# Performance work log

Measured on AMD Instinct MI355X. Metric: run time of the kernel, lower is better.

Reference implementation:

```python
import jax, jax.numpy as jnp
import numpy as np

T = 65536
INPUT_SIZE = 128
HIDDEN = 100
OUT = 1


def setup_inputs() -> dict:
    key = jax.random.key(0)
    ks = jax.random.split(key, 8)
    s = 1.0 / np.sqrt(HIDDEN)  # PyTorch LSTM/Linear init bound
    u = lambda k, shape: jax.random.uniform(k, shape, jnp.float32, -s, s)
    return {
        "input_x": jax.random.normal(ks[0], (T, INPUT_SIZE), jnp.float32),
        "W_ih": u(ks[1], (4 * HIDDEN, INPUT_SIZE)),
        "W_hh": u(ks[2], (4 * HIDDEN, HIDDEN)),
        "b_ih": u(ks[3], (4 * HIDDEN,)),
        "b_hh": u(ks[4], (4 * HIDDEN,)),
        "W_lin": u(ks[5], (OUT, HIDDEN)),
        "b_lin": u(ks[6], (OUT,)),
    }


def reference(input_x, W_ih, W_hh, b_ih, b_hh, W_lin, b_lin):
    H = W_hh.shape[1]
    # batch=1: squeeze it away; precompute input projections for all timesteps
    x_proj = input_x @ W_ih.T + (b_ih + b_hh)  # [T, 4H]

    def step(carry, xp):
        h, c = carry
        gates = xp + h @ W_hh.T  # [4H]
        i, f, g, o = jnp.split(gates, 4)
        i = jax.nn.sigmoid(i)
        f = jax.nn.sigmoid(f)
        g = jnp.tanh(g)
        o = jax.nn.sigmoid(o)
        c = f * c + i * g
        h = o * jnp.tanh(c)
        return (h, c), h

    h0 = jnp.zeros((H,), input_x.dtype)
    c0 = jnp.zeros((H,), input_x.dtype)
    _, hs = jax.lax.scan(step, (h0, c0), x_proj)  # hs: [T, H]
    predictions = jax.nn.sigmoid(hs @ W_lin.T + b_lin)  # [T, 1]
    return predictions
```

## Files before the change

### kernel.cpp

```cpp
#include <hip/hip_runtime.h>
#include <hip/hip_bf16.h>

#define TSEQ 65536
#define INPUT_SIZE 128
#define HIDDEN 100
#define GATES 400

typedef __attribute__((ext_vector_type(8))) short bf16x8;
typedef __attribute__((ext_vector_type(4))) float f32x4;

__device__ __forceinline__ unsigned short f2bf(float x) {
    union { float f; unsigned int u; } v; v.f = x;
    unsigned int r = v.u + 0x7fffu + ((v.u >> 16) & 1u);
    return (unsigned short)(r >> 16);
}
__device__ __forceinline__ unsigned short f2bf_fast(float x) {
    unsigned int r;
    asm("v_cvt_pk_bf16_f32 %0, %1, %2" : "=v"(r) : "v"(x), "v"(0.0f));
    return (unsigned short)r;
}
__device__ __forceinline__ float bf2f(unsigned int u) {
    union { unsigned int u; float f; } v; v.u = u << 16; return v.f;
}
__device__ __forceinline__ float rcp_fast(float x) { return __builtin_amdgcn_rcpf(x); }
__device__ __forceinline__ float sigm(float x) { return rcp_fast(1.0f + __expf(-x)); }

template <int CTRL>
__device__ __forceinline__ float qb(float v) {
    int i = __builtin_bit_cast(int, v);
    int r = __builtin_amdgcn_mov_dpp(i, CTRL, 0xF, 0xF, true);
    return __builtin_bit_cast(float, r);
}

#define LDS_BARRIER()                                              \
    do {                                                           \
        asm volatile("s_waitcnt lgkmcnt(0)" ::: "memory");         \
        __builtin_amdgcn_s_barrier();                              \
        asm volatile("" ::: "memory");                             \
    } while (0)

__global__ __launch_bounds__(256) void xproj_kernel(
    const float* __restrict__ x,
    const float* __restrict__ W,
    const float* __restrict__ bi,
    const float* __restrict__ bh,
    float* __restrict__ xp)
{
    __shared__ __align__(16) float xs[16 * 128];
    const int tid = threadIdx.x;
    const int t0 = blockIdx.x * 16;

#pragma unroll
    for (int i = 0; i < 8; ++i)
        xs[i * 256 + tid] = x[(size_t)t0 * 128 + i * 256 + tid];
    __syncthreads();

    const int j1 = tid;
    const int j2 = tid + 256;
    const bool has2 = (j2 < GATES);
    const int u1 = j1 % 100, g1 = j1 / 100;
    const int p1 = 16 * (u1 >> 2) + 4 * (u1 & 3) + g1;
    const int u2 = has2 ? (j2 % 100) : 0, g2 = has2 ? (j2 / 100) : 0;
    const int p2 = 16 * (u2 >> 2) + 4 * (u2 & 3) + g2;

    float acc1[16], acc2[16];
    const float bias1 = bi[j1] + bh[j1];
    const float bias2 = has2 ? (bi[j2] + bh[j2]) : 0.0f;
#pragma unroll
    for (int tt = 0; tt < 16; ++tt) { acc1[tt] = bias1; acc2[tt] = bias2; }

    const float4* W4 = reinterpret_cast<const float4*>(W);
    const float4* xs4 = reinterpret_cast<const float4*>(xs);

    for (int kk = 0; kk < 32; ++kk) {
        const float4 wa = W4[(size_t)j1 * 32 + kk];
        float4 wb = make_float4(0.f, 0.f, 0.f, 0.f);
        if (has2) wb = W4[(size_t)j2 * 32 + kk];
#pragma unroll
        for (int tt = 0; tt < 16; ++tt) {
            const float4 xv = xs4[tt * 32 + kk];
            acc1[tt] = fmaf(wa.x, xv.x, acc1[tt]);
            acc1[tt] = fmaf(wa.y, xv.y, acc1[tt]);
            acc1[tt] = fmaf(wa.z, xv.z, acc1[tt]);
            acc1[tt] = fmaf(wa.w, xv.w, acc1[tt]);
            acc2[tt] = fmaf(wb.x, xv.x, acc2[tt]);
            acc2[tt] = fmaf(wb.y, xv.y, acc2[tt]);
            acc2[tt] = fmaf(wb.z, xv.z, acc2[tt]);
            acc2[tt] = fmaf(wb.w, xv.w, acc2[tt]);
        }
    }

#pragma unroll
    for (int tt = 0; tt < 16; ++tt) {
        xp[(size_t)(t0 + tt) * GATES + p1] = acc1[tt];
        if (has2) xp[(size_t)(t0 + tt) * GATES + p2] = acc2[tt];
    }
}

__global__ __launch_bounds__(512, 1) void lstm_rec_kernel(
    const float* __restrict__ xp,
    const float* __restrict__ Whh,
    unsigned short* __restrict__ hs)
{
    __shared__ __align__(16) unsigned short h_lds[2][128];

    const int tid = threadIdx.x;
    const int lane = tid & 63;
    const int w = tid >> 6;
    const int bq = lane >> 4;
    const int m = lane & 15;
    const int g = m & 3;

    bf16x8 wfrag[4][4];
#pragma unroll
    for (int i = 0; i < 4; ++i) {
        const int ti = (i < 3) ? (3 * w + i) : 24;
        const bool valid = (i < 3) || (w == 7);
        const int uu = 4 * ti + (m >> 2);
        const int orow = g * 100 + uu;
#pragma unroll
        for (int kk = 0; kk < 4; ++kk) {
            float vals[8];
            if (valid && kk < 3) {
                const float4 w0 = *(const float4*)&Whh[(size_t)orow * 100 + kk * 32 + bq * 8];
                const float4 w1 = *(const float4*)&Whh[(size_t)orow * 100 + kk * 32 + bq * 8 + 4];
                vals[0] = w0.x; vals[1] = w0.y; vals[2] = w0.z; vals[3] = w0.w;
                vals[4] = w1.x; vals[5] = w1.y; vals[6] = w1.z; vals[7] = w1.w;
            } else if (valid && bq == 0) {
                const float4 w0 = *(const float4*)&Whh[(size_t)orow * 100 + 96];
                vals[0] = w0.x; vals[1] = w0.y; vals[2] = w0.z; vals[3] = w0.w;
                vals[4] = 0.f; vals[5] = 0.f; vals[6] = 0.f; vals[7] = 0.f;
            } else {
#pragma unroll
                for (int j = 0; j < 8; ++j) vals[j] = 0.f;
            }
#pragma unroll
            for (int j = 0; j < 8; ++j) wfrag[i][kk][j] = (short)f2bf(vals[j]);
        }
    }

    const int mytile = (bq < 3) ? (3 * w + bq) : 24;
    const int unit = 4 * mytile + (m >> 2);
    const int pown = 16 * mytile + m;
    const bool qvalid = (bq < 3) || (w == 7);
    const bool writer = qvalid && (g == 3);
    const float kk2 = (g == 2) ? 2.0f : 1.0f;
    const float bsub = (g == 2) ? 2.0f : 1.0f;
    const bool isg1 = (g == 1);

    if (tid < 128) { h_lds[0][tid] = 0; h_lds[1][tid] = 0; }
    float c = 0.0f;
    float xqv[4];
#pragma unroll
    for (int p = 0; p < 4; ++p)
        xqv[p] = xp[(size_t)p * GATES + pown];
    __syncthreads();

    for (int t = 0; t < TSEQ; t += 4) {
#pragma unroll
        for (int u = 0; u < 4; ++u) {
            const int tt = t + u;
            const int cur = u & 1;

            bf16x8 bfr[4];
#pragma unroll
            for (int kk = 0; kk < 4; ++kk) {
                const uint4 braw = *(const uint4*)&h_lds[cur][kk * 32 + bq * 8];
                bfr[kk] = __builtin_bit_cast(bf16x8, braw);
            }

            f32x4 acc_s[4];
#pragma unroll
            for (int i = 0; i < 4; ++i) {
                if (i < 3 || w == 7) {
                    f32x4 acc = {0.f, 0.f, 0.f, 0.f};
                    acc = __builtin_amdgcn_mfma_f32_16x16x32_bf16(bfr[0], wfrag[i][0], acc, 0, 0, 0);
                    acc = __builtin_amdgcn_mfma_f32_16x16x32_bf16(bfr[1], wfrag[i][1], acc, 0, 0, 0);
                    acc = __builtin_amdgcn_mfma_f32_16x16x32_bf16(bfr[2], wfrag[i][2], acc, 0, 0, 0);
                    acc = __builtin_amdgcn_mfma_f32_16x16x32_bf16(bfr[3], wfrag[i][3], acc, 0, 0, 0);
                    acc_s[i] = acc;
                } else {
                    acc_s[i] = (f32x4){0.f, 0.f, 0.f, 0.f};
                }
            }

            float pre = acc_s[0][0];
            pre = (bq == 1) ? acc_s[1][0] : pre;
            pre = (bq == 2) ? acc_s[2][0] : pre;
            pre = (bq == 3) ? acc_s[3][0] : pre;
            pre += xqv[u];

            const float e = __expf(pre * kk2);
            const float act = fmaf(-bsub, rcp_fast(e + 1.0f), 1.0f);

            const float prod = act * qb<0xAA>(act);
            const float cnew = fmaf(act, c, qb<0x00>(prod));
            c = isg1 ? cnew : c;
            const float e2 = __expf(c + c);
            const float tc = fmaf(-2.0f, rcp_fast(e2 + 1.0f), 1.0f);
            const float hv = act * qb<0x55>(tc);
            const unsigned short hb = f2bf_fast(hv);

            if (writer) {
                h_lds[1 - cur][unit] = hb;
                hs[(size_t)tt * HIDDEN + unit] = hb;
            }
            xqv[u] = xp[(size_t)(tt + 4) * GATES + pown];

            LDS_BARRIER();
        }
    }
}

__global__ __launch_bounds__(256) void pred_kernel(
    const unsigned short* __restrict__ hs,
    const float* __restrict__ wlin,
    const float* __restrict__ blin,
    float* __restrict__ out)
{
    __shared__ __align__(16) float wl[HIDDEN];
    const int tid = threadIdx.x;
    if (tid < HIDDEN) wl[tid] = wlin[tid];
    __syncthreads();

    const int t = blockIdx.x * 256 + tid;
    const unsigned short* hrow = hs + (size_t)t * HIDDEN;
    float acc = blin[0];
#pragma unroll
    for (int kk = 0; kk < 25; ++kk) {
        const uint2 v = *(const uint2*)&hrow[kk * 4];
        acc = fmaf(bf2f(v.x & 0xffffu), wl[kk * 4 + 0], acc);
        acc = fmaf(bf2f(v.x >> 16),     wl[kk * 4 + 1], acc);
        acc = fmaf(bf2f(v.y & 0xffffu), wl[kk * 4 + 2], acc);
        acc = fmaf(bf2f(v.y >> 16),     wl[kk * 4 + 3], acc);
    }
    out[t] = sigm(acc);
}

extern "C" void kernel_launch(void* const* d_in, const int* in_sizes, int n_in,
                              void* d_out, int out_size, void* d_ws, size_t ws_size,
                              hipStream_t stream) {
    const float* x     = (const float*)d_in[0];
    const float* W_ih  = (const float*)d_in[1];
    const float* W_hh  = (const float*)d_in[2];
    const float* b_ih  = (const float*)d_in[3];
    const float* b_hh  = (const float*)d_in[4];
    const float* W_lin = (const float*)d_in[5];
    const float* b_lin = (const float*)d_in[6];
    float* out = (float*)d_out;

    float* xp = (float*)d_ws;
    unsigned short* hs = (unsigned short*)(xp + (size_t)TSEQ * GATES);

    xproj_kernel<<<TSEQ / 16, 256, 0, stream>>>(x, W_ih, b_ih, b_hh, xp);
    lstm_rec_kernel<<<1, 512, 0, stream>>>(xp, W_hh, hs);
    pred_kernel<<<TSEQ / 256, 256, 0, stream>>>(hs, W_lin, b_lin, out);
}
```

Baseline: 23.44 ms.

## Replace MFMA recurrent matvec with per-lane fp16 dot2 over register-resident weights

The per-step recurrent matvec moves off MFMA tiles and onto plain VALU work. Each lane owns one gate row of W_hh, held in 50 fp16x2 registers, and computes its dot product against the whole h vector read from LDS using v_dot2 instructions. The hidden state and the stored hs switch from bf16 to fp16, and the xproj output layout becomes a simple 4*unit+gate interleave. The aim is to cut per-step MFMA latency and the lane-select overhead on the serial critical path. The cost is 13 LDS vector reads per lane per step and a longer serial dot2 chain.

```diff
diff --git a/kernel.cpp b/kernel.cpp
--- a/kernel.cpp
+++ b/kernel.cpp
@@ -6,24 +6,20 @@
 #define HIDDEN 100
 #define GATES 400
 
-typedef __attribute__((ext_vector_type(8))) short bf16x8;
-typedef __attribute__((ext_vector_type(4))) float f32x4;
-
-__device__ __forceinline__ unsigned short f2bf(float x) {
-    union { float f; unsigned int u; } v; v.f = x;
-    unsigned int r = v.u + 0x7fffu + ((v.u >> 16) & 1u);
-    return (unsigned short)(r >> 16);
-}
-__device__ __forceinline__ unsigned short f2bf_fast(float x) {
-    unsigned int r;
-    asm("v_cvt_pk_bf16_f32 %0, %1, %2" : "=v"(r) : "v"(x), "v"(0.0f));
-    return (unsigned short)r;
-}
-__device__ __forceinline__ float bf2f(unsigned int u) {
-    union { unsigned int u; float f; } v; v.u = u << 16; return v.f;
-}
+typedef __fp16 __attribute__((ext_vector_type(2))) f16x2;
+
 __device__ __forceinline__ float rcp_fast(float x) { return __builtin_amdgcn_rcpf(x); }
 __device__ __forceinline__ float sigm(float x) { return rcp_fast(1.0f + __expf(-x)); }
+
+#if __has_builtin(__builtin_amdgcn_fdot2)
+__device__ __forceinline__ float dot2(f16x2 a, f16x2 b, float c) {
+    return __builtin_amdgcn_fdot2(a, b, c, false);
+}
+#else
+__device__ __forceinline__ float dot2(f16x2 a, f16x2 b, float c) {
+    return fmaf((float)a.x, (float)b.x, fmaf((float)a.y, (float)b.y, c));
+}
+#endif
 
 template <int CTRL>
 __device__ __forceinline__ float qb(float v) {
@@ -58,10 +54,8 @@
     const int j1 = tid;
     const int j2 = tid + 256;
     const bool has2 = (j2 < GATES);
-    const int u1 = j1 % 100, g1 = j1 / 100;
-    const int p1 = 16 * (u1 >> 2) + 4 * (u1 & 3) + g1;
-    const int u2 = has2 ? (j2 % 100) : 0, g2 = has2 ? (j2 / 100) : 0;
-    const int p2 = 16 * (u2 >> 2) + 4 * (u2 & 3) + g2;
+    const int p1 = 4 * (j1 % 100) + (j1 / 100);
+    const int p2 = has2 ? (4 * (j2 % 100) + (j2 / 100)) : 0;
 
     float acc1[16], acc2[16];
     const float bias1 = bi[j1] + bh[j1];
@@ -107,88 +101,70 @@
     const int tid = threadIdx.x;
     const int lane = tid & 63;
     const int w = tid >> 6;
-    const int bq = lane >> 4;
-    const int m = lane & 15;
-    const int g = m & 3;
-
-    bf16x8 wfrag[4][4];
-#pragma unroll
-    for (int i = 0; i < 4; ++i) {
-        const int ti = (i < 3) ? (3 * w + i) : 24;
-        const bool valid = (i < 3) || (w == 7);
-        const int uu = 4 * ti + (m >> 2);
-        const int orow = g * 100 + uu;
-#pragma unroll
-        for (int kk = 0; kk < 4; ++kk) {
-            float vals[8];
-            if (valid && kk < 3) {
-                const float4 w0 = *(const float4*)&Whh[(size_t)orow * 100 + kk * 32 + bq * 8];
-                const float4 w1 = *(const float4*)&Whh[(size_t)orow * 100 + kk * 32 + bq * 8 + 4];
-                vals[0] = w0.x; vals[1] = w0.y; vals[2] = w0.z; vals[3] = w0.w;
-                vals[4] = w1.x; vals[5] = w1.y; vals[6] = w1.z; vals[7] = w1.w;
-            } else if (valid && bq == 0) {
-                const float4 w0 = *(const float4*)&Whh[(size_t)orow * 100 + 96];
-                vals[0] = w0.x; vals[1] = w0.y; vals[2] = w0.z; vals[3] = w0.w;
-                vals[4] = 0.f; vals[5] = 0.f; vals[6] = 0.f; vals[7] = 0.f;
-            } else {
-#pragma unroll
-                for (int j = 0; j < 8; ++j) vals[j] = 0.f;
-            }
-#pragma unroll
-            for (int j = 0; j < 8; ++j) wfrag[i][kk][j] = (short)f2bf(vals[j]);
+    const int ubase = (w < 4) ? 13 * w : 52 + 12 * (w - 4);
+    const int ucnt = (w < 4) ? 13 : 12;
+    const bool act_lane = lane < 4 * ucnt;
+    const int g = lane & 3;
+    const int unit = act_lane ? (ubase + (lane >> 2)) : 0;
+    const int p = 4 * unit + g;
+    const int orow = g * 100 + unit;
+
+    f16x2 wreg[50];
+    if (act_lane) {
+        const float4* wr = reinterpret_cast<const float4*>(Whh + (size_t)orow * 100);
+#pragma unroll
+        for (int kk = 0; kk < 25; ++kk) {
+            const float4 v = wr[kk];
+            wreg[2 * kk]     = f16x2{(__fp16)v.x, (__fp16)v.y};
+            wreg[2 * kk + 1] = f16x2{(__fp16)v.z, (__fp16)v.w};
         }
-    }
-
-    const int mytile = (bq < 3) ? (3 * w + bq) : 24;
-    const int unit = 4 * mytile + (m >> 2);
-    const int pown = 16 * mytile + m;
-    const bool qvalid = (bq < 3) || (w == 7);
-    const bool writer = qvalid && (g == 3);
+    } else {
+#pragma unroll
+        for (int j = 0; j < 50; ++j) wreg[j] = f16x2{(__fp16)0.f, (__fp16)0.f};
+    }
+
+    const bool writer = act_lane && (g == 3);
     const float kk2 = (g == 2) ? 2.0f : 1.0f;
     const float bsub = (g == 2) ? 2.0f : 1.0f;
     const bool isg1 = (g == 1);
 
     if (tid < 128) { h_lds[0][tid] = 0; h_lds[1][tid] = 0; }
     float c = 0.0f;
+    const float* xq_ptr = xp + p;
     float xqv[4];
 #pragma unroll
-    for (int p = 0; p < 4; ++p)
-        xqv[p] = xp[(size_t)p * GATES + pown];
+    for (int pp = 0; pp < 4; ++pp) xqv[pp] = xq_ptr[pp * GATES];
+    xq_ptr += 4 * GATES;
+    unsigned short* hp = hs + unit;
     __syncthreads();
 
     for (int t = 0; t < TSEQ; t += 4) {
 #pragma unroll
         for (int u = 0; u < 4; ++u) {
-            const int tt = t + u;
             const int cur = u & 1;
 
-            bf16x8 bfr[4];
-#pragma unroll
-            for (int kk = 0; kk < 4; ++kk) {
-                const uint4 braw = *(const uint4*)&h_lds[cur][kk * 32 + bq * 8];
-                bfr[kk] = __builtin_bit_cast(bf16x8, braw);
+            unsigned hw[52];
+#pragma unroll
+            for (int r = 0; r < 13; ++r) {
+                const uint4 q = *(const uint4*)&h_lds[cur][r * 8];
+                hw[4 * r + 0] = q.x; hw[4 * r + 1] = q.y;
+                hw[4 * r + 2] = q.z; hw[4 * r + 3] = q.w;
             }
 
-            f32x4 acc_s[4];
-#pragma unroll
-            for (int i = 0; i < 4; ++i) {
-                if (i < 3 || w == 7) {
-                    f32x4 acc = {0.f, 0.f, 0.f, 0.f};
-                    acc = __builtin_amdgcn_mfma_f32_16x16x32_bf16(bfr[0], wfrag[i][0], acc, 0, 0, 0);
-                    acc = __builtin_amdgcn_mfma_f32_16x16x32_bf16(bfr[1], wfrag[i][1], acc, 0, 0, 0);
-                    acc = __builtin_amdgcn_mfma_f32_16x16x32_bf16(bfr[2], wfrag[i][2], acc, 0, 0, 0);
-                    acc = __builtin_amdgcn_mfma_f32_16x16x32_bf16(bfr[3], wfrag[i][3], acc, 0, 0, 0);
-                    acc_s[i] = acc;
-                } else {
-                    acc_s[i] = (f32x4){0.f, 0.f, 0.f, 0.f};
-                }
-            }
-
-            float pre = acc_s[0][0];
-            pre = (bq == 1) ? acc_s[1][0] : pre;
-            pre = (bq == 2) ? acc_s[2][0] : pre;
-            pre = (bq == 3) ? acc_s[3][0] : pre;
-            pre += xqv[u];
+            float a0 = 0.f, a1 = 0.f, a2 = 0.f, a3 = 0.f;
+#pragma unroll
+            for (int j = 0; j < 13; ++j)
+                a0 = dot2(wreg[j], __builtin_bit_cast(f16x2, hw[j]), a0);
+#pragma unroll
+            for (int j = 13; j < 26; ++j)
+                a1 = dot2(wreg[j], __builtin_bit_cast(f16x2, hw[j]), a1);
+#pragma unroll
+            for (int j = 26; j < 38; ++j)
+                a2 = dot2(wreg[j], __builtin_bit_cast(f16x2, hw[j]), a2);
+#pragma unroll
+            for (int j = 38; j < 50; ++j)
+                a3 = dot2(wreg[j], __builtin_bit_cast(f16x2, hw[j]), a3);
+            const float pre = ((a0 + a1) + (a2 + a3)) + xqv[u];
 
             const float e = __expf(pre * kk2);
             const float act = fmaf(-bsub, rcp_fast(e + 1.0f), 1.0f);
@@ -199,16 +175,19 @@
             const float e2 = __expf(c + c);
             const float tc = fmaf(-2.0f, rcp_fast(e2 + 1.0f), 1.0f);
             const float hv = act * qb<0x55>(tc);
-            const unsigned short hb = f2bf_fast(hv);
+            union { __fp16 h; unsigned short u16; } cv;
+            cv.h = (__fp16)hv;
 
             if (writer) {
-                h_lds[1 - cur][unit] = hb;
-                hs[(size_t)tt * HIDDEN + unit] = hb;
+                h_lds[1 - cur][unit] = cv.u16;
+                hp[u * HIDDEN] = cv.u16;
             }
-            xqv[u] = xp[(size_t)(tt + 4) * GATES + pown];
+            xqv[u] = xq_ptr[u * GATES];
 
             LDS_BARRIER();
         }
+        xq_ptr += 4 * GATES;
+        hp += 4 * HIDDEN;
     }
 }
 
@@ -229,10 +208,12 @@
 #pragma unroll
     for (int kk = 0; kk < 25; ++kk) {
         const uint2 v = *(const uint2*)&hrow[kk * 4];
-        acc = fmaf(bf2f(v.x & 0xffffu), wl[kk * 4 + 0], acc);
-        acc = fmaf(bf2f(v.x >> 16),     wl[kk * 4 + 1], acc);
-        acc = fmaf(bf2f(v.y & 0xffffu), wl[kk * 4 + 2], acc);
-        acc = fmaf(bf2f(v.y >> 16),     wl[kk * 4 + 3], acc);
+        const f16x2 h01 = __builtin_bit_cast(f16x2, v.x);
+        const f16x2 h23 = __builtin_bit_cast(f16x2, v.y);
+        acc = fmaf((float)h01.x, wl[kk * 4 + 0], acc);
+        acc = fmaf((float)h01.y, wl[kk * 4 + 1], acc);
+        acc = fmaf((float)h23.x, wl[kk * 4 + 2], acc);
+        acc = fmaf((float)h23.y, wl[kk * 4 + 3], acc);
     }
     out[t] = sigm(acc);
 }
```

Measured after the change: 29.00 ms. +23.7%, slower.
